# Kernel tuning notes

Hardware: AMD Instinct MI355X
Metric: run time of the kernel (lower is better)

The kernel has to match this reference:

```python
import jax, jax.numpy as jnp
import numpy as np


def setup_inputs() -> dict:
    key = jax.random.key(0)
    k1, k2, k3 = jax.random.split(key, 3)
    b, c, h, w = 4, 64, 64, 64
    content = jax.random.normal(k1, (b, c, h, w), dtype=jnp.float32)
    content_s = jax.random.normal(k2, (b, c, h, w), dtype=jnp.float32)
    style = jax.random.normal(k3, (b, c, h, w), dtype=jnp.float32)
    return {"content": content, "content_s": content_s, "style": style}


def reference(content, content_s, style):
    b, c, h, w = content.shape
    hw = h * w
    Fc = content.reshape(b, c, hw)      # [b, c, HW]
    Fs = content_s.reshape(b, c, hw)    # [b, c, HW]
    Fst = style.reshape(b, c, hw)       # [b, c, HW]
    # S[b, q, k] = sum_c Fc[b, c, q] * Fs[b, c, k]  (Fc transposed as in torch)
    S = jnp.einsum('bcq,bck->bqk', Fc, Fs)
    S = jax.nn.softmax(S, axis=-1)
    # O = style @ S^T : O[b, c, q] = sum_k Fst[b, c, k] * S[b, q, k]
    O = jnp.einsum('bck,bqk->bcq', Fst, S).reshape(b, c, h, w)
    return jnp.concatenate((content, O), axis=1)
```

## Files before the change

### kernel.cpp

```cpp
#include <hip/hip_runtime.h>
#include <math.h>


#define Bb 4
#define Cc 64
#define HWs 4096
#define RLOG2E 1.44269504088896340736f
#define DEFER_THR 6.0f

typedef _Float16 half8 __attribute__((ext_vector_type(8)));
typedef _Float16 half4 __attribute__((ext_vector_type(4)));
typedef float floatx4 __attribute__((ext_vector_type(4)));
typedef unsigned uint2v __attribute__((ext_vector_type(2)));

#define GAS __attribute__((address_space(1)))
#define LAS __attribute__((address_space(3)))

extern "C" __device__ float __ocml_native_exp2_f32(float);
#if defined(__has_builtin) && __has_builtin(__builtin_amdgcn_exp2f)
#define EXP2(x) __builtin_amdgcn_exp2f(x)
#else
#define EXP2(x) __ocml_native_exp2_f32(x)
#endif

__global__ __launch_bounds__(256) void prep_k(const float* __restrict__ content,
                                              const float* __restrict__ Fs,
                                              const float* __restrict__ Fst,
                                              float* __restrict__ out,
                                              _Float16* __restrict__ Kt,
                                              _Float16* __restrict__ Vt) {
    const int bid = blockIdx.x;
    const int t = threadIdx.x;
    if (bid < 1024) {
        int i4 = bid * 256 + t;
        const float4* c4 = (const float4*)content;
        const float4* v4 = (const float4*)Fst;
        float4* o4 = (float4*)out;
        int b = i4 >> 16, rem = i4 & 65535;
        o4[(size_t)b * 131072 + rem] = c4[i4];
        float4 v = v4[i4];
        half4 h;
        h[0] = (_Float16)v.x; h[1] = (_Float16)v.y;
        h[2] = (_Float16)v.z; h[3] = (_Float16)v.w;
        *(half4*)(Vt + (size_t)i4 * 4) = h;
    } else {
        __shared__ _Float16 T[16][72];
        int e = bid - 1024;
        int b = e >> 8;
        int hw0 = (e & 255) * 16;
        const float* sb = Fs + (size_t)b * Cc * HWs;
        {
            int c = t >> 2, x4 = (t & 3) * 4;
            float4 v = *(const float4*)(sb + (size_t)c * HWs + hw0 + x4);
            T[x4 + 0][c] = (_Float16)v.x;
            T[x4 + 1][c] = (_Float16)v.y;
            T[x4 + 2][c] = (_Float16)v.z;
            T[x4 + 3][c] = (_Float16)v.w;
        }
        __syncthreads();
        if (t < 128) {
            int row = t >> 3, g = t & 7;
            _Float16* db = Kt + (size_t)b * HWs * Cc;
            *(half8*)(db + (size_t)(hw0 + row) * Cc + g * 8) = *(half8*)&T[row][g * 8];
        }
    }
}

template <int NS>
__global__ __launch_bounds__(256, 2) void attn_k(const float* __restrict__ Fc,
                                                 const _Float16* __restrict__ Kt,
                                                 const _Float16* __restrict__ Vt,
                                                 _Float16* __restrict__ Opart,
                                                 float2* __restrict__ ml) {
    constexpr int TPS = 64 / NS;
    const int tid  = threadIdx.x;
    const int lane = tid & 63;
    const int quad = lane >> 4;
    const int l15  = lane & 15;
    const int w    = tid >> 6;
    const int qg = blockIdx.x & 15;
    const int b  = (blockIdx.x >> 4) & 3;
    const int s  = blockIdx.x >> 6;
    const int k0base = s * TPS * 64;
    const int qbase = qg * 256 + w * 64 + l15;

    __shared__ _Float16 Kl[3][64 * 64];
    __shared__ _Float16 Vl[3][64 * 64];

    const float*    Fcb = Fc + (size_t)b * Cc * HWs;
    const _Float16* Kb  = Kt + (size_t)b * HWs * Cc;
    const _Float16* Vb  = Vt + (size_t)b * Cc * HWs;

    const int lrow = lane >> 3;
    const int lj   = lane & 7;
    const int lsw8 = (lj ^ lrow) * 8;
    const int r0   = w * 16;

    auto stage = [&](int kt) {
        const int kk0 = k0base + kt * 64;
        #pragma unroll
        for (int c = 0; c < 2; ++c) {
            const int r = r0 + c * 8 + lrow;
            __builtin_amdgcn_global_load_lds(
                (const GAS void*)(Kb + (size_t)(kk0 + r) * 64 + lsw8),
                (LAS void*)&Kl[kt % 3][(r0 + c * 8) * 64], 16, 0, 0);
            __builtin_amdgcn_global_load_lds(
                (const GAS void*)(Vb + (size_t)r * HWs + kk0 + lsw8),
                (LAS void*)&Vl[kt % 3][(r0 + c * 8) * 64], 16, 0, 0);
        }
    };

    half8 qf[4][2];
    #pragma unroll
    for (int g = 0; g < 4; ++g) {
        const int q = qbase + g * 16;
        #pragma unroll
        for (int j = 0; j < 8; ++j) {
            qf[g][0][j] = (_Float16)(Fcb[(size_t)(quad * 8 + j) * HWs + q] * RLOG2E);
            qf[g][1][j] = (_Float16)(Fcb[(size_t)(32 + quad * 8 + j) * HWs + q] * RLOG2E);
        }
    }

    floatx4 acc[4][4];
    floatx4 accl[4];
    float m_run[4];
    #pragma unroll
    for (int g = 0; g < 4; ++g) {
        accl[g] = (floatx4)(0.0f);
        m_run[g] = 0.0f;
        #pragma unroll
        for (int m = 0; m < 4; ++m) acc[g][m] = (floatx4)(0.0f);
    }

    half8 vone;
    #pragma unroll
    for (int j = 0; j < 8; ++j) vone[j] = (_Float16)1.0f;

    asm volatile("" ::: "memory");
    stage(0);
    stage(1);

    const int swl = l15 & 7;
    const int o0 = (quad ^ swl) * 8;
    const int o1 = ((4 + quad) ^ swl) * 8;

    #pragma unroll
    for (int kt = 0; kt < TPS; ++kt) {
        const int p = kt % 3;
        if (kt + 1 < TPS) asm volatile("s_waitcnt vmcnt(4)" ::: "memory");
        else              asm volatile("s_waitcnt vmcnt(0)" ::: "memory");
        __builtin_amdgcn_s_barrier();
        __builtin_amdgcn_sched_barrier(0);
        if (kt + 2 < TPS) stage(kt + 2);

        floatx4 sv[4][4];
        #pragma unroll
        for (int m = 0; m < 4; ++m) {
            const half8 ka0 = *(const half8*)&Kl[p][(m * 16 + l15) * 64 + o0];
            const half8 ka1 = *(const half8*)&Kl[p][(m * 16 + l15) * 64 + o1];
            #pragma unroll
            for (int g = 0; g < 4; ++g) {
                sv[g][m] = __builtin_amdgcn_mfma_f32_16x16x32_f16(ka0, qf[g][0], (floatx4)(-m_run[g]), 0, 0, 0);
                sv[g][m] = __builtin_amdgcn_mfma_f32_16x16x32_f16(ka1, qf[g][1], sv[g][m], 0, 0, 0);
            }
        }

        half8 pb[4][2];
        #pragma unroll
        for (int g = 0; g < 4; ++g) {
            float mm0 = fmaxf(fmaxf(fmaxf(sv[g][0][0], sv[g][0][1]), sv[g][0][2]), sv[g][0][3]);
            float mm1 = fmaxf(fmaxf(fmaxf(sv[g][1][0], sv[g][1][1]), sv[g][1][2]), sv[g][1][3]);
            float mm2 = fmaxf(fmaxf(fmaxf(sv[g][2][0], sv[g][2][1]), sv[g][2][2]), sv[g][2][3]);
            float mm3 = fmaxf(fmaxf(fmaxf(sv[g][3][0], sv[g][3][1]), sv[g][3][2]), sv[g][3][3]);
            float mx = fmaxf(fmaxf(fmaxf(mm0, mm1), mm2), mm3);
            if (!__all(mx <= DEFER_THR)) {
                unsigned mu = __float_as_uint(mx);
                uint2v t32 = __builtin_amdgcn_permlane32_swap(mu, mu, false, false);
                float wmx = fmaxf(__uint_as_float(t32[0]), __uint_as_float(t32[1]));
                mu = __float_as_uint(wmx);
                uint2v t16 = __builtin_amdgcn_permlane16_swap(mu, mu, false, false);
                wmx = fmaxf(__uint_as_float(t16[0]), __uint_as_float(t16[1]));
                float delta = fmaxf(wmx, 0.0f);
                float alpha = EXP2(-delta);
                m_run[g] += delta;
                #pragma unroll
                for (int m = 0; m < 4; ++m) acc[g][m] *= alpha;
                accl[g] *= alpha;
                #pragma unroll
                for (int m = 0; m < 4; ++m)
                    #pragma unroll
                    for (int r = 0; r < 4; ++r) sv[g][m][r] -= delta;
            }
            unsigned Ap[4], Bp[4];
            #pragma unroll
            for (int m = 0; m < 4; ++m) {
                float e0 = EXP2(sv[g][m][0]);
                float e1 = EXP2(sv[g][m][1]);
                float e2 = EXP2(sv[g][m][2]);
                float e3 = EXP2(sv[g][m][3]);
                Ap[m] = __builtin_bit_cast(unsigned, __builtin_amdgcn_cvt_pkrtz(e0, e1));
                Bp[m] = __builtin_bit_cast(unsigned, __builtin_amdgcn_cvt_pkrtz(e2, e3));
            }
            unsigned pw[2][4];
            { uint2v a = __builtin_amdgcn_permlane32_swap(Ap[0], Ap[1], false, false);
              uint2v u = __builtin_amdgcn_permlane16_swap(a[0], a[1], false, false);
              pw[0][0] = u[0]; pw[0][2] = u[1]; }
            { uint2v a = __builtin_amdgcn_permlane32_swap(Bp[0], Bp[1], false, false);
              uint2v u = __builtin_amdgcn_permlane16_swap(a[0], a[1], false, false);
              pw[0][1] = u[0]; pw[0][3] = u[1]; }
            { uint2v a = __builtin_amdgcn_permlane32_swap(Ap[2], Ap[3], false, false);
              uint2v u = __builtin_amdgcn_permlane16_swap(a[0], a[1], false, false);
              pw[1][0] = u[0]; pw[1][2] = u[1]; }
            { uint2v a = __builtin_amdgcn_permlane32_swap(Bp[2], Bp[3], false, false);
              uint2v u = __builtin_amdgcn_permlane16_swap(a[0], a[1], false, false);
              pw[1][1] = u[0]; pw[1][3] = u[1]; }
            #pragma unroll
            for (int ks = 0; ks < 2; ++ks) {
                union { unsigned u4[4]; half8 h; } z;
                z.u4[0] = pw[ks][0]; z.u4[1] = pw[ks][1];
                z.u4[2] = pw[ks][2]; z.u4[3] = pw[ks][3];
                pb[g][ks] = z.h;
            }
        }

        #pragma unroll
        for (int m = 0; m < 4; ++m) {
            const half8 va0 = *(const half8*)&Vl[p][(m * 16 + l15) * 64 + o0];
            const half8 va1 = *(const half8*)&Vl[p][(m * 16 + l15) * 64 + o1];
            #pragma unroll
            for (int g = 0; g < 4; ++g) {
                acc[g][m] = __builtin_amdgcn_mfma_f32_16x16x32_f16(va0, pb[g][0], acc[g][m], 0, 0, 0);
                acc[g][m] = __builtin_amdgcn_mfma_f32_16x16x32_f16(va1, pb[g][1], acc[g][m], 0, 0, 0);
            }
        }
        #pragma unroll
        for (int g = 0; g < 4; ++g) {
            accl[g] = __builtin_amdgcn_mfma_f32_16x16x32_f16(vone, pb[g][0], accl[g], 0, 0, 0);
            accl[g] = __builtin_amdgcn_mfma_f32_16x16x32_f16(vone, pb[g][1], accl[g], 0, 0, 0);
        }
    }

    _Float16* op = Opart + (((size_t)s * Bb + b) * Cc) * HWs;
    #pragma unroll
    for (int g = 0; g < 4; ++g) {
        const int q = qbase + g * 16;
        #pragma unroll
        for (int m = 0; m < 4; ++m)
            #pragma unroll
            for (int r = 0; r < 4; ++r) {
                int c = m * 16 + quad * 4 + r;
                op[(size_t)c * HWs + q] = (_Float16)acc[g][m][r];
            }
        if (quad == 0)
            ml[((size_t)b * HWs + q) * NS + s] = make_float2(m_run[g], accl[g][0]);
    }
}

template <int NS>
__global__ __launch_bounds__(256) void combine_k(const _Float16* __restrict__ Opart,
                                                 const float2* __restrict__ ml,
                                                 float* __restrict__ out) {
    int idx = blockIdx.x * 256 + threadIdx.x;
    int q = idx & 4095;
    int c = (idx >> 12) & 63;
    int b = idx >> 18;
    const float2* mlp = ml + ((size_t)b * HWs + q) * NS;
    float2 mls[NS];
    #pragma unroll
    for (int s = 0; s < NS; ++s) mls[s] = mlp[s];
    float M = -INFINITY;
    #pragma unroll
    for (int s = 0; s < NS; ++s) M = fmaxf(M, mls[s].x);
    float l = 0.0f, o = 0.0f;
    #pragma unroll
    for (int s = 0; s < NS; ++s) {
        float wgt = EXP2(mls[s].x - M);
        l += wgt * mls[s].y;
        o += wgt * (float)Opart[(((size_t)s * Bb + b) * Cc + c) * HWs + q];
    }
    out[((size_t)b * 2 * Cc + Cc + c) * HWs + q] = o / l;
}

extern "C" void kernel_launch(void* const* d_in, const int* in_sizes, int n_in,
                              void* d_out, int out_size, void* d_ws, size_t ws_size,
                              hipStream_t stream) {
    const float* content   = (const float*)d_in[0];
    const float* content_s = (const float*)d_in[1];
    const float* style     = (const float*)d_in[2];
    float* out = (float*)d_out;

    _Float16* Kt = (_Float16*)d_ws;
    _Float16* Vt = Kt + (size_t)Bb * HWs * Cc;
    _Float16* Opart = Vt + (size_t)Bb * Cc * HWs;

    const size_t base = (size_t)2 * Bb * HWs * Cc * sizeof(_Float16);
    const size_t need8 = base + (size_t)8 * Bb * Cc * HWs * sizeof(_Float16)
                              + (size_t)Bb * HWs * 8 * sizeof(float2);
    const int ns = (ws_size >= need8) ? 8 : 4;
    float2* ml = (float2*)(Opart + (size_t)ns * Bb * Cc * HWs);

    prep_k<<<dim3(2048), dim3(256), 0, stream>>>(content, content_s, style, out, Kt, Vt);
    if (ns == 8) {
        attn_k<8><<<dim3(8 * Bb * 16), dim3(256), 0, stream>>>(content, Kt, Vt, Opart, ml);
        combine_k<8><<<dim3(4096), dim3(256), 0, stream>>>(Opart, ml, out);
    } else {
        attn_k<4><<<dim3(4 * Bb * 16), dim3(256), 0, stream>>>(content, Kt, Vt, Opart, ml);
        combine_k<4><<<dim3(4096), dim3(256), 0, stream>>>(Opart, ml, out);
    }
}
```

Measured before the change: 103.6 us.

## Restructure attention tile loop per query group and stop unrolling the key-tile loop

Loads all K and V fragments from LDS up front, then processes each of the four query groups end to end (QK MFMA, softmax, PV MFMA) instead of doing all QK for every group first. This shrinks live score registers from 4x4 floatx4 down to 4, and lets one group's exp and permlane work interleave with other groups' MFMAs. The outer key-tile loop changes to unroll 1, which cuts code size but adds loop overhead and a runtime modulo for the LDS buffer index. Serial per-group dependencies may leave less independent MFMA work for the scheduler.

```diff
diff --git a/kernel.cpp b/kernel.cpp
--- a/kernel.cpp
+++ b/kernel.cpp
@@ -144,7 +144,7 @@
     const int o0 = (quad ^ swl) * 8;
     const int o1 = ((4 + quad) ^ swl) * 8;
 
-    #pragma unroll
+    #pragma unroll 1
     for (int kt = 0; kt < TPS; ++kt) {
         const int p = kt % 3;
         if (kt + 1 < TPS) asm volatile("s_waitcnt vmcnt(4)" ::: "memory");
@@ -153,25 +153,30 @@
         __builtin_amdgcn_sched_barrier(0);
         if (kt + 2 < TPS) stage(kt + 2);
 
-        floatx4 sv[4][4];
+        half8 ka[4][2], va[4][2];
         #pragma unroll
         for (int m = 0; m < 4; ++m) {
-            const half8 ka0 = *(const half8*)&Kl[p][(m * 16 + l15) * 64 + o0];
-            const half8 ka1 = *(const half8*)&Kl[p][(m * 16 + l15) * 64 + o1];
+            const _Float16* row = &Kl[p][(m * 16 + l15) * 64];
+            ka[m][0] = *(const half8*)(row + o0);
+            ka[m][1] = *(const half8*)(row + o1);
+            const _Float16* vrow = &Vl[p][(m * 16 + l15) * 64];
+            va[m][0] = *(const half8*)(vrow + o0);
+            va[m][1] = *(const half8*)(vrow + o1);
+        }
+
+        #pragma unroll
+        for (int g = 0; g < 4; ++g) {
+            floatx4 sv[4];
             #pragma unroll
-            for (int g = 0; g < 4; ++g) {
-                sv[g][m] = __builtin_amdgcn_mfma_f32_16x16x32_f16(ka0, qf[g][0], (floatx4)(-m_run[g]), 0, 0, 0);
-                sv[g][m] = __builtin_amdgcn_mfma_f32_16x16x32_f16(ka1, qf[g][1], sv[g][m], 0, 0, 0);
-            }
-        }
-
-        half8 pb[4][2];
-        #pragma unroll
-        for (int g = 0; g < 4; ++g) {
-            float mm0 = fmaxf(fmaxf(fmaxf(sv[g][0][0], sv[g][0][1]), sv[g][0][2]), sv[g][0][3]);
-            float mm1 = fmaxf(fmaxf(fmaxf(sv[g][1][0], sv[g][1][1]), sv[g][1][2]), sv[g][1][3]);
-            float mm2 = fmaxf(fmaxf(fmaxf(sv[g][2][0], sv[g][2][1]), sv[g][2][2]), sv[g][2][3]);
-            float mm3 = fmaxf(fmaxf(fmaxf(sv[g][3][0], sv[g][3][1]), sv[g][3][2]), sv[g][3][3]);
+            for (int m = 0; m < 4; ++m) {
+                sv[m] = __builtin_amdgcn_mfma_f32_16x16x32_f16(ka[m][0], qf[g][0], (floatx4)(-m_run[g]), 0, 0, 0);
+                sv[m] = __builtin_amdgcn_mfma_f32_16x16x32_f16(ka[m][1], qf[g][1], sv[m], 0, 0, 0);
+            }
+
+            float mm0 = fmaxf(fmaxf(fmaxf(sv[0][0], sv[0][1]), sv[0][2]), sv[0][3]);
+            float mm1 = fmaxf(fmaxf(fmaxf(sv[1][0], sv[1][1]), sv[1][2]), sv[1][3]);
+            float mm2 = fmaxf(fmaxf(fmaxf(sv[2][0], sv[2][1]), sv[2][2]), sv[2][3]);
+            float mm3 = fmaxf(fmaxf(fmaxf(sv[3][0], sv[3][1]), sv[3][2]), sv[3][3]);
             float mx = fmaxf(fmaxf(fmaxf(mm0, mm1), mm2), mm3);
             if (!__all(mx <= DEFER_THR)) {
                 unsigned mu = __float_as_uint(mx);
@@ -189,15 +194,15 @@
                 #pragma unroll
                 for (int m = 0; m < 4; ++m)
                     #pragma unroll
-                    for (int r = 0; r < 4; ++r) sv[g][m][r] -= delta;
+                    for (int r = 0; r < 4; ++r) sv[m][r] -= delta;
             }
             unsigned Ap[4], Bp[4];
             #pragma unroll
             for (int m = 0; m < 4; ++m) {
-                float e0 = EXP2(sv[g][m][0]);
-                float e1 = EXP2(sv[g][m][1]);
-                float e2 = EXP2(sv[g][m][2]);
-                float e3 = EXP2(sv[g][m][3]);
+                float e0 = EXP2(sv[m][0]);
+                float e1 = EXP2(sv[m][1]);
+                float e2 = EXP2(sv[m][2]);
+                float e3 = EXP2(sv[m][3]);
                 Ap[m] = __builtin_bit_cast(unsigned, __builtin_amdgcn_cvt_pkrtz(e0, e1));
                 Bp[m] = __builtin_bit_cast(unsigned, __builtin_amdgcn_cvt_pkrtz(e2, e3));
             }
@@ -214,29 +219,24 @@
             { uint2v a = __builtin_amdgcn_permlane32_swap(Bp[2], Bp[3], false, false);
               uint2v u = __builtin_amdgcn_permlane16_swap(a[0], a[1], false, false);
               pw[1][1] = u[0]; pw[1][3] = u[1]; }
+            half8 pb0, pb1;
+            {
+                union { unsigned u4[4]; half8 h; } z;
+                z.u4[0] = pw[0][0]; z.u4[1] = pw[0][1];
+                z.u4[2] = pw[0][2]; z.u4[3] = pw[0][3];
+                pb0 = z.h;
+                z.u4[0] = pw[1][0]; z.u4[1] = pw[1][1];
+                z.u4[2] = pw[1][2]; z.u4[3] = pw[1][3];
+                pb1 = z.h;
+            }
+
             #pragma unroll
-            for (int ks = 0; ks < 2; ++ks) {
-                union { unsigned u4[4]; half8 h; } z;
-                z.u4[0] = pw[ks][0]; z.u4[1] = pw[ks][1];
-                z.u4[2] = pw[ks][2]; z.u4[3] = pw[ks][3];
-                pb[g][ks] = z.h;
-            }
-        }
-
-        #pragma unroll
-        for (int m = 0; m < 4; ++m) {
-            const half8 va0 = *(const half8*)&Vl[p][(m * 16 + l15) * 64 + o0];
-            const half8 va1 = *(const half8*)&Vl[p][(m * 16 + l15) * 64 + o1];
-            #pragma unroll
-            for (int g = 0; g < 4; ++g) {
-                acc[g][m] = __builtin_amdgcn_mfma_f32_16x16x32_f16(va0, pb[g][0], acc[g][m], 0, 0, 0);
-                acc[g][m] = __builtin_amdgcn_mfma_f32_16x16x32_f16(va1, pb[g][1], acc[g][m], 0, 0, 0);
-            }
-        }
-        #pragma unroll
-        for (int g = 0; g < 4; ++g) {
-            accl[g] = __builtin_amdgcn_mfma_f32_16x16x32_f16(vone, pb[g][0], accl[g], 0, 0, 0);
-            accl[g] = __builtin_amdgcn_mfma_f32_16x16x32_f16(vone, pb[g][1], accl[g], 0, 0, 0);
+            for (int m = 0; m < 4; ++m) {
+                acc[g][m] = __builtin_amdgcn_mfma_f32_16x16x32_f16(va[m][0], pb0, acc[g][m], 0, 0, 0);
+                acc[g][m] = __builtin_amdgcn_mfma_f32_16x16x32_f16(va[m][1], pb1, acc[g][m], 0, 0, 0);
+            }
+            accl[g] = __builtin_amdgcn_mfma_f32_16x16x32_f16(vone, pb0, accl[g], 0, 0, 0);
+            accl[g] = __builtin_amdgcn_mfma_f32_16x16x32_f16(vone, pb1, accl[g], 0, 0, 0);
         }
     }
 
```

Measured after the change: 105.3 us. Within noise of the previous version (+1.7%).
